# Kernel tuning notes

Hardware: AMD Instinct MI355X
Metric: run time of the kernel (lower is better)

Reference implementation:

```python
import jax, jax.numpy as jnp
import numpy as np

HIDDEN = 2048
Q_HEADS = 16
KV_HEADS = 4
HEAD_DIM = HIDDEN // Q_HEADS  # 128
GROUPS = Q_HEADS // KV_HEADS  # 4


def setup_inputs() -> dict:
    key = jax.random.key(0)
    ks = jax.random.split(key, 5)
    scale = 1.0 / np.sqrt(HIDDEN)
    x = jax.random.normal(ks[0], (1, 4096, HIDDEN), dtype=jnp.float32)
    # nn.Linear weights stored as [out_features, in_features]
    Wq = jax.random.uniform(ks[1], (Q_HEADS * HEAD_DIM, HIDDEN), jnp.float32, -scale, scale)
    Wk = jax.random.uniform(ks[2], (KV_HEADS * HEAD_DIM, HIDDEN), jnp.float32, -scale, scale)
    Wv = jax.random.uniform(ks[3], (KV_HEADS * HEAD_DIM, HIDDEN), jnp.float32, -scale, scale)
    Wo = jax.random.uniform(ks[4], (HIDDEN, HIDDEN), jnp.float32, -scale, scale)
    return {"x": x, "Wq": Wq, "Wk": Wk, "Wv": Wv, "Wo": Wo}


def reference(x, Wq, Wk, Wv, Wo):
    b, s, _ = x.shape
    norm = jnp.asarray(np.sqrt(HEAD_DIM), x.dtype)
    # Projections (Linear without bias: x @ W.T)
    q = (x @ Wq.T).reshape(b, s, KV_HEADS, GROUPS, HEAD_DIM)  # group q heads by shared kv head
    k = (x @ Wk.T).reshape(b, s, KV_HEADS, HEAD_DIM)
    v = (x @ Wv.T).reshape(b, s, KV_HEADS, HEAD_DIM)
    # Scores: repeat_interleave of KV is equivalent to sharing k across the g axis
    att = jnp.einsum('bskgd,btkd->bkgst', q, k) / norm  # [b,kv,groups,s,s]
    att = jax.nn.softmax(att, axis=-1)
    out = jnp.einsum('bkgst,btkd->bskgd', att, v).reshape(b, s, HIDDEN)
    return out @ Wo.T
```

## Files before the change

kernel.cpp:

```cpp
#include <hip/hip_runtime.h>
#include <stdint.h>

#define SEQ 4096
#define HID 2048

typedef __attribute__((ext_vector_type(8))) short short8;
typedef __attribute__((ext_vector_type(4))) float f32x4;
typedef __attribute__((ext_vector_type(16))) float f32x16;
typedef unsigned int u32;
typedef __attribute__((ext_vector_type(4))) u32 u32x4;

__device__ __forceinline__ short bf16_rne(float f) {
  u32 u = __builtin_bit_cast(u32, f);
  u += 0x7FFFu + ((u >> 16) & 1u);
  return (short)(u >> 16);
}

__device__ __forceinline__ void gload16(const void* gp, void* lp) {
  __builtin_amdgcn_global_load_lds(
      (const __attribute__((address_space(1))) u32*)(uintptr_t)gp,
      (__attribute__((address_space(3))) u32*)(uintptr_t)lp, 16, 0, 0);
}

__global__ __launch_bounds__(256) void cast_all(const float* __restrict__ x,
                                                const float* __restrict__ Wq,
                                                const float* __restrict__ Wk,
                                                const float* __restrict__ Wv,
                                                const float* __restrict__ Wo,
                                                short* __restrict__ xb,
                                                short* __restrict__ wqkv,
                                                short* __restrict__ wob, float qscale) {
  int i = blockIdx.x * 256 + threadIdx.x;
  const float* src;
  short* dst;
  float s = 1.0f;
  int off;
  if (i < 1048576) {
    src = x; dst = xb; off = i;
  } else if (i < 1572864) {
    src = Wq; dst = wqkv; off = i - 1048576; s = qscale;
  } else if (i < 1703936) {
    src = Wk; dst = wqkv + (size_t)2048 * 2048; off = i - 1572864;
  } else if (i < 1835008) {
    src = Wv; dst = wqkv + (size_t)2560 * 2048; off = i - 1703936;
  } else {
    src = Wo; dst = wob; off = i - 1835008;
  }
  const f32x4* p = (const f32x4*)src + (size_t)off * 2;
  f32x4 a = p[0], b = p[1];
  short8 o;
#pragma unroll
  for (int j = 0; j < 4; ++j) { o[j] = bf16_rne(a[j] * s); o[j + 4] = bf16_rne(b[j] * s); }
  *((short8*)dst + off) = o;
}

template <typename CT, bool FUSE_VT>
__global__ __launch_bounds__(256, 2) void gemm_nt(const short* __restrict__ A,
                                                  const short* __restrict__ B,
                                                  CT* __restrict__ C, int M, int N, int K,
                                                  short* __restrict__ vt) {
  __shared__ __align__(16) short As[128 * 32];
  __shared__ __align__(16) short Bs[128 * 32];
  int tid = threadIdx.x, wave = tid >> 6, lane = tid & 63;
  int lr = lane & 15, lg = lane >> 4;
  int wr = wave >> 1, wc = wave & 1;
  size_t rowA0 = (size_t)blockIdx.y * 128, colB0 = (size_t)blockIdx.x * 128;
  f32x4 acc[4][4] = {};

  for (int kt = 0; kt < K; kt += 32) {
#pragma unroll
    for (int c = 0; c < 2; ++c) {
      int chunk = wave * 2 + c;
      int row = chunk * 16 + (lane >> 2);
      int col = (lane & 3) * 8;
      gload16(A + (rowA0 + row) * (size_t)K + kt + col, &As[chunk * 512]);
      gload16(B + (colB0 + row) * (size_t)K + kt + col, &Bs[chunk * 512]);
    }
    __syncthreads();
    short8 a[4], b[4];
#pragma unroll
    for (int i = 0; i < 4; ++i) {
      a[i] = *(const short8*)&As[(wr * 64 + i * 16 + lr) * 32 + lg * 8];
      b[i] = *(const short8*)&Bs[(wc * 64 + i * 16 + lr) * 32 + lg * 8];
    }
#pragma unroll
    for (int i = 0; i < 4; ++i)
#pragma unroll
      for (int j = 0; j < 4; ++j)
        acc[i][j] = __builtin_amdgcn_mfma_f32_16x16x32_bf16(a[i], b[j], acc[i][j], 0, 0, 0);
    __syncthreads();
  }

  if constexpr (FUSE_VT) {
    if (colB0 >= 2560) {
      int lgp = ((lg & 1) << 1) | (lg >> 1);
#pragma unroll
      for (int i = 0; i < 4; ++i)
#pragma unroll
        for (int j = 0; j < 4; ++j)
#pragma unroll
          for (int r = 0; r < 4; ++r) {
            size_t d = colB0 - 2560 + wc * 64 + j * 16 + lr;
            size_t pos = rowA0 + wr * 64 + i * 16 + lgp * 4 + r;
            vt[d * SEQ + pos] = bf16_rne(acc[i][j][r]);
          }
      return;
    }
  }
#pragma unroll
  for (int i = 0; i < 4; ++i)
#pragma unroll
    for (int j = 0; j < 4; ++j)
#pragma unroll
      for (int r = 0; r < 4; ++r) {
        size_t row = rowA0 + wr * 64 + i * 16 + lg * 4 + r;
        size_t col = colB0 + wc * 64 + j * 16 + lr;
        if constexpr (sizeof(CT) == 2) C[row * N + col] = (CT)bf16_rne(acc[i][j][r]);
        else C[row * N + col] = acc[i][j][r];
      }
}

__global__ __launch_bounds__(256, 2) void attn_kernel(const short* __restrict__ QKV,
                                                      const short* __restrict__ Vt,
                                                      short* __restrict__ Oat) {
  __shared__ __align__(16) short Ks[2][4096];
  __shared__ __align__(16) short Vs[2][4096];
  int tid = threadIdx.x, wave = tid >> 6, lane = tid & 63;
  int l31 = lane & 31, hi = lane >> 5;
  int h = blockIdx.y, kv = h >> 2;
  int q0 = blockIdx.x * 128 + wave * 32;

  short8 qf[8];
#pragma unroll
  for (int kb = 0; kb < 8; ++kb)
    qf[kb] = *(const short8*)&QKV[(size_t)(q0 + l31) * 3072 + h * 128 + kb * 16 + hi * 8];

  f32x16 oacc[4] = {};
  float lsum = 0.f;

  const short* Kbase = QKV + 2048 + kv * 128;

  auto stageK = [&](int b, int t0) {
#pragma unroll
    for (int cc = 0; cc < 2; ++cc) {
      int c = wave * 2 + cc;
      gload16(Kbase + (size_t)(t0 + l31) * 3072 + c * 16 + hi * 8, &Ks[b][c * 512]);
    }
  };
  auto stageV = [&](int b, int t0) {
#pragma unroll
    for (int cc = 0; cc < 2; ++cc) {
      int c = wave * 2 + cc;
      int d = (c & 1) * 64 + lane;
      gload16(Vt + (size_t)(kv * 128 + d) * SEQ + t0 + (c >> 1) * 8, &Vs[b][c * 512]);
    }
  };

  stageK(0, 0);
  stageV(0, 0);
  __syncthreads();
  int buf = 0;

  for (int t0 = 0; t0 < SEQ; t0 += 32) {
    int tn = (t0 + 32 < SEQ) ? t0 + 32 : 0;
    stageK(buf ^ 1, tn);
    stageV(buf ^ 1, tn);

    f32x16 sa = {}, sb = {};
    __builtin_amdgcn_s_setprio(1);
#pragma unroll
    for (int kb = 0; kb < 4; ++kb) {
      short8 kfa = *(const short8*)&Ks[buf][((kb * 2 + hi) * 32 + l31) * 8];
      short8 kfb = *(const short8*)&Ks[buf][(((kb + 4) * 2 + hi) * 32 + l31) * 8];
      sa = __builtin_amdgcn_mfma_f32_32x32x16_bf16(kfa, qf[kb], sa, 0, 0, 0);
      sb = __builtin_amdgcn_mfma_f32_32x32x16_bf16(kfb, qf[kb + 4], sb, 0, 0, 0);
    }
    __builtin_amdgcn_s_setprio(0);

    float pp[8];
    u32 w[8];
#pragma unroll
    for (int ii = 0; ii < 8; ++ii) {
      float p0 = __builtin_amdgcn_exp2f(sa[2 * ii] + sb[2 * ii]);
      float p1 = __builtin_amdgcn_exp2f(sa[2 * ii + 1] + sb[2 * ii + 1]);
      pp[ii] = p0 + p1;
      asm("v_cvt_pk_bf16_f32 %0, %1, %2" : "=v"(w[ii]) : "v"(p0), "v"(p1));
    }
    lsum += ((pp[0] + pp[1]) + (pp[2] + pp[3])) + ((pp[4] + pp[5]) + (pp[6] + pp[7]));
    short8 pa0 = __builtin_bit_cast(short8, (u32x4){w[0], w[1], w[2], w[3]});
    short8 pa1 = __builtin_bit_cast(short8, (u32x4){w[4], w[5], w[6], w[7]});

    __builtin_amdgcn_s_setprio(1);
#pragma unroll
    for (int nb = 0; nb < 4; ++nb) {
      short8 v0 = *(const short8*)&Vs[buf][((hi)*128 + nb * 32 + l31) * 8];
      oacc[nb] = __builtin_amdgcn_mfma_f32_32x32x16_bf16(pa0, v0, oacc[nb], 0, 0, 0);
    }
#pragma unroll
    for (int nb = 0; nb < 4; ++nb) {
      short8 v1 = *(const short8*)&Vs[buf][((2 + hi) * 128 + nb * 32 + l31) * 8];
      oacc[nb] = __builtin_amdgcn_mfma_f32_32x32x16_bf16(pa1, v1, oacc[nb], 0, 0, 0);
    }
    __builtin_amdgcn_s_setprio(0);

    __syncthreads();
    buf ^= 1;
  }

  lsum += __shfl_xor(lsum, 32);
  float linv = 1.f / lsum;
#pragma unroll
  for (int r = 0; r < 16; ++r) {
    int qrow = (r & 3) + 8 * (r >> 2) + 4 * hi;
    float lr_ = __shfl(linv, qrow);
#pragma unroll
    for (int nb = 0; nb < 4; ++nb)
      Oat[(size_t)(q0 + qrow) * HID + h * 128 + nb * 32 + l31] = bf16_rne(oacc[nb][r] * lr_);
  }
}

extern "C" void kernel_launch(void* const* d_in, const int* in_sizes, int n_in,
                              void* d_out, int out_size, void* d_ws, size_t ws_size,
                              hipStream_t stream) {
  const float* x = (const float*)d_in[0];
  const float* Wq = (const float*)d_in[1];
  const float* Wk = (const float*)d_in[2];
  const float* Wv = (const float*)d_in[3];
  const float* Wo = (const float*)d_in[4];
  float* out = (float*)d_out;
  char* ws = (char*)d_ws;

  short* xb = (short*)(ws);
  short* wqkv = (short*)(ws + (16u << 20));
  short* wob = (short*)(ws + (28u << 20));
  short* qkv = (short*)(ws + (36u << 20));
  short* vt = (short*)(ws + (60u << 20));
  short* oat = xb;

  const float QSCALE = 0.12753102964551932f;

  cast_all<<<9216, 256, 0, stream>>>(x, Wq, Wk, Wv, Wo, xb, wqkv, wob, QSCALE);

  gemm_nt<short, true><<<dim3(24, 32), 256, 0, stream>>>(xb, wqkv, qkv, 4096, 3072, 2048, vt);
  attn_kernel<<<dim3(32, 16), 256, 0, stream>>>(qkv, vt, oat);
  gemm_nt<float, false><<<dim3(16, 32), 256, 0, stream>>>(oat, wob, out, 4096, HID, 2048,
                                                          nullptr);
}
```

Before: 269.0 us.

## Split attention KV range into three parts and merge partial outputs

```diff
diff --git a/kernel.cpp b/kernel.cpp
--- a/kernel.cpp
+++ b/kernel.cpp
@@ -5,6 +5,7 @@
 #define HID 2048
 
 typedef __attribute__((ext_vector_type(8))) short short8;
+typedef __attribute__((ext_vector_type(8))) _Float16 half8;
 typedef __attribute__((ext_vector_type(4))) float f32x4;
 typedef __attribute__((ext_vector_type(16))) float f32x16;
 typedef unsigned int u32;
@@ -120,14 +121,17 @@
       }
 }
 
-__global__ __launch_bounds__(256, 2) void attn_kernel(const short* __restrict__ QKV,
-                                                      const short* __restrict__ Vt,
-                                                      short* __restrict__ Oat) {
+template <int NSPLIT>
+__global__ __launch_bounds__(256, NSPLIT == 3 ? 3 : 2)
+void attn_kernel(const short* __restrict__ QKV, const short* __restrict__ Vt,
+                 short* __restrict__ Oat, _Float16* __restrict__ op0,
+                 _Float16* __restrict__ opart, short* __restrict__ mlhole) {
   __shared__ __align__(16) short Ks[2][4096];
   __shared__ __align__(16) short Vs[2][4096];
   int tid = threadIdx.x, wave = tid >> 6, lane = tid & 63;
   int l31 = lane & 31, hi = lane >> 5;
   int h = blockIdx.y, kv = h >> 2;
+  int part = (NSPLIT == 3) ? blockIdx.z : 0;
   int q0 = blockIdx.x * 128 + wave * 32;
 
   short8 qf[8];
@@ -156,13 +160,16 @@
     }
   };
 
-  stageK(0, 0);
-  stageV(0, 0);
+  const int tbeg = (NSPLIT == 3) ? part * 1376 : 0;
+  const int tend = (NSPLIT == 3) ? ((part == 2) ? SEQ : tbeg + 1376) : SEQ;
+
+  stageK(0, tbeg);
+  stageV(0, tbeg);
   __syncthreads();
   int buf = 0;
 
-  for (int t0 = 0; t0 < SEQ; t0 += 32) {
-    int tn = (t0 + 32 < SEQ) ? t0 + 32 : 0;
+  for (int t0 = tbeg; t0 < tend; t0 += 32) {
+    int tn = (t0 + 32 < tend) ? t0 + 32 : tbeg;
     stageK(buf ^ 1, tn);
     stageV(buf ^ 1, tn);
 
@@ -208,15 +215,53 @@
   }
 
   lsum += __shfl_xor(lsum, 32);
-  float linv = 1.f / lsum;
-#pragma unroll
-  for (int r = 0; r < 16; ++r) {
-    int qrow = (r & 3) + 8 * (r >> 2) + 4 * hi;
-    float lr_ = __shfl(linv, qrow);
-#pragma unroll
-    for (int nb = 0; nb < 4; ++nb)
-      Oat[(size_t)(q0 + qrow) * HID + h * 128 + nb * 32 + l31] = bf16_rne(oacc[nb][r] * lr_);
-  }
+
+  if constexpr (NSPLIT == 1) {
+    float linv = 1.f / lsum;
+#pragma unroll
+    for (int r = 0; r < 16; ++r) {
+      int qrow = (r & 3) + 8 * (r >> 2) + 4 * hi;
+      float lr_ = __shfl(linv, qrow);
+#pragma unroll
+      for (int nb = 0; nb < 4; ++nb)
+        Oat[(size_t)(q0 + qrow) * HID + h * 128 + nb * 32 + l31] = bf16_rne(oacc[nb][r] * lr_);
+    }
+  } else {
+    _Float16* Obase = (part == 0) ? op0 : opart + (size_t)(part - 1) * SEQ * HID;
+#pragma unroll
+    for (int r = 0; r < 16; ++r) {
+      int qrow = (r & 3) + 8 * (r >> 2) + 4 * hi;
+#pragma unroll
+      for (int nb = 0; nb < 4; ++nb)
+        Obase[(size_t)(q0 + qrow) * HID + h * 128 + nb * 32 + l31] = (_Float16)oacc[nb][r];
+    }
+    if (hi == 0) {
+      float* mlq = (float*)(mlhole + (size_t)(q0 + l31) * 3072 + 2560);
+      mlq[h * 3 + part] = lsum;
+    }
+  }
+}
+
+__global__ __launch_bounds__(256) void merge3(const _Float16* __restrict__ op0,
+                                              const _Float16* __restrict__ op1,
+                                              const _Float16* __restrict__ op2,
+                                              const short* __restrict__ qkvml,
+                                              short* __restrict__ Oat) {
+  int i = blockIdx.x * 256 + threadIdx.x;
+  int row = i >> 8;
+  int col = (i & 255) * 8;
+  int h = col >> 7;
+  const float* mlq = (const float*)(qkvml + (size_t)row * 3072 + 2560);
+  float inv = 1.f / (mlq[h * 3] + mlq[h * 3 + 1] + mlq[h * 3 + 2]);
+  size_t idx = (size_t)row * HID + col;
+  half8 a = *(const half8*)&op0[idx];
+  half8 b = *(const half8*)&op1[idx];
+  half8 c = *(const half8*)&op2[idx];
+  short8 o;
+#pragma unroll
+  for (int j = 0; j < 8; ++j)
+    o[j] = bf16_rne(((float)a[j] + (float)b[j] + (float)c[j]) * inv);
+  *(short8*)&Oat[idx] = o;
 }
 
 extern "C" void kernel_launch(void* const* d_in, const int* in_sizes, int n_in,
@@ -236,13 +281,23 @@
   short* qkv = (short*)(ws + (36u << 20));
   short* vt = (short*)(ws + (60u << 20));
   short* oat = xb;
+  _Float16* op0 = (_Float16*)xb;
+  _Float16* op1 = (_Float16*)(ws + (64u << 20));
+  _Float16* op2 = (_Float16*)(ws + (80u << 20));
+  const bool split3 = ws_size >= ((size_t)96u << 20);
 
   const float QSCALE = 0.12753102964551932f;
 
   cast_all<<<9216, 256, 0, stream>>>(x, Wq, Wk, Wv, Wo, xb, wqkv, wob, QSCALE);
 
   gemm_nt<short, true><<<dim3(24, 32), 256, 0, stream>>>(xb, wqkv, qkv, 4096, 3072, 2048, vt);
-  attn_kernel<<<dim3(32, 16), 256, 0, stream>>>(qkv, vt, oat);
+
+  if (split3) {
+    attn_kernel<3><<<dim3(32, 16, 3), 256, 0, stream>>>(qkv, vt, nullptr, op0, op1, qkv);
+    merge3<<<4096, 256, 0, stream>>>(op0, op1, op2, qkv, oat);
+  } else {
+    attn_kernel<1><<<dim3(32, 16, 1), 256, 0, stream>>>(qkv, vt, oat, nullptr, nullptr, nullptr);
+  }
   gemm_nt<float, false><<<dim3(16, 32), 256, 0, stream>>>(oat, wob, out, 4096, HID, 2048,
                                                           nullptr);
 }
```

New measurement: 290.4 us. 1.08x slower.
